# Kernel optimization log

Measured on AMD Instinct MI355X. Metric: run time of the kernel, lower is better.

Reference implementation:

```python
import jax, jax.numpy as jnp
import numpy as np

EPS = 1e-5


def _bn(h, gamma, beta):
    # BatchNorm1d, training mode: biased batch statistics over nodes
    mu = jnp.mean(h, axis=0)
    var = jnp.mean(jnp.square(h - mu), axis=0)
    return (h - mu) * jax.lax.rsqrt(var + EPS) * gamma + beta


def setup_inputs() -> dict:
    key = jax.random.key(0)
    ks = jax.random.split(key, 12)
    N, E, D, H = 50000, 800000, 128, 256
    x = jax.random.normal(ks[0], (N, D), dtype=jnp.float32)
    edge_index = jax.random.randint(ks[1], (2, E), 0, N, dtype=jnp.int64)
    train_node_id = jax.random.randint(ks[2], (10000,), 0, N, dtype=jnp.int64)
    def lin(k, fan_in, fan_out):
        bound = 1.0 / np.sqrt(fan_in)
        return jax.random.uniform(k, (fan_in, fan_out), jnp.float32, -bound, bound)
    return {
        "x": x, "edge_index": edge_index, "train_node_id": train_node_id,
        "W1": lin(ks[3], D, H), "b1": jnp.zeros((H,), jnp.float32),
        "W2": lin(ks[4], H, H), "b2": jnp.zeros((H,), jnp.float32),
        "W3": lin(ks[5], H, H), "b3": jnp.zeros((H,), jnp.float32),
        "g1": jnp.ones((H,), jnp.float32), "be1": jnp.zeros((H,), jnp.float32),
        "g2": jnp.ones((H,), jnp.float32), "be2": jnp.zeros((H,), jnp.float32),
        "g3": jnp.ones((H,), jnp.float32), "be3": jnp.zeros((H,), jnp.float32),
        "Wl": lin(ks[6], H, H), "bl": jnp.zeros((H,), jnp.float32),
        "Wf": lin(ks[7], H, 1), "bf": jnp.zeros((1,), jnp.float32),
    }


def reference(x, edge_index, train_node_id, W1, b1, W2, b2, W3, b3,
              g1, be1, g2, be2, g3, be3, Wl, bl, Wf, bf):
    N = x.shape[0]
    loops = jnp.arange(N, dtype=edge_index.dtype)
    row = jnp.concatenate([edge_index[0], loops])  # destinations
    col = jnp.concatenate([edge_index[1], loops])  # sources
    deg = jax.ops.segment_sum(jnp.ones_like(row, dtype=x.dtype), row, num_segments=N)
    d_isqrt = jax.lax.rsqrt(deg)  # deg >= 1 due to self loops
    norm = (d_isqrt[row] * d_isqrt[col])[:, None]  # [E+N, 1]

    def gcn(h, W, b):
        hW = h @ W
        agg = jax.ops.segment_sum(hW[col] * norm, row, num_segments=N)
        return agg + b

    h = jax.nn.relu(_bn(gcn(x, W1, b1), g1, be1))
    h = jax.nn.relu(_bn(gcn(h, W2, b2), g2, be2))
    h = jax.nn.relu(_bn(gcn(h, W3, b3), g3, be3))
    h = jax.nn.relu(h @ Wl + bl)
    h = h[train_node_id]
    return jnp.squeeze(h @ Wf + bf, -1)
```

## Files before the change

### kernel.cpp

```cpp
#include <hip/hip_runtime.h>

typedef unsigned short u16;
typedef unsigned char u8;
typedef __attribute__((ext_vector_type(8))) short short8;
typedef __attribute__((ext_vector_type(4))) float f32x4;

#define GPB 25
#define SCAP 8

#define DEVFN static __device__ __forceinline__

DEVFN u16 f2b(float f) {
    union { float f; unsigned v; } x; x.f = f;
    unsigned r = x.v + 0x7fffu + ((x.v >> 16) & 1u);
    return (u16)(r >> 16);
}

DEVFN int detect64(const int* __restrict__ p) {
    int orv = 0;
#pragma unroll
    for (int i = 1; i < 64; i += 2) orv |= p[i];
    return (orv == 0) ? 1 : 0;
}

DEVFN unsigned get_xcc() {
    unsigned x;
    asm volatile("s_getreg_b32 %0, hwreg(HW_REG_XCC_ID)" : "=s"(x));
    return x & 7u;
}

DEVFN void accum_row8(short8 v, float* acc) {
    const unsigned* u = (const unsigned*)&v;
#pragma unroll
    for (int k = 0; k < 4; k++) {
        union { float f; unsigned w; } lo, hi;
        lo.w = u[k] << 16;
        hi.w = u[k] & 0xffff0000u;
        acc[2 * k] += lo.f;
        acc[2 * k + 1] += hi.f;
    }
}

__global__ void k_init(const float* __restrict__ W1, const float* __restrict__ W2,
                       const float* __restrict__ W3, const float* __restrict__ Wl,
                       u16* __restrict__ T1, u16* __restrict__ T2,
                       u16* __restrict__ T3, u16* __restrict__ Tl,
                       int* __restrict__ z9,
                       float* __restrict__ stat, float* __restrict__ out, int N, int M) {
    int t = blockIdx.x * 256 + threadIdx.x;
    int Z = (N * 9) / 4;
    if (t < 229376) {
        const float* W; u16* T; int K; int idx;
        if (t < 32768)        { W = W1; T = T1; K = 128; idx = t; }
        else if (t < 98304)   { W = W2; T = T2; K = 256; idx = t - 32768; }
        else if (t < 163840)  { W = W3; T = T3; K = 256; idx = t - 98304; }
        else                  { W = Wl; T = Tl; K = 256; idx = t - 163840; }
        int k = idx >> 8, n = idx & 255;
        T[(size_t)n * K + k] = f2b(W[(size_t)k * 256 + n]);
    } else if (t < 229376 + Z) {
        ((int4*)z9)[t - 229376] = (int4){0, 0, 0, 0};
    } else if (t < 229376 + Z + 384) {
        ((float4*)stat)[t - 229376 - Z] = (float4){0.f, 0.f, 0.f, 0.f};
    } else if (t < 229376 + Z + 384 + (M + 3) / 4) {
        int i = (t - 229376 - Z - 384) * 4;
        if (i + 3 < M) *(float4*)(out + i) = (float4){0.f, 0.f, 0.f, 0.f};
        else for (int k = i; k < M; k++) out[k] = 0.f;
    }
}

__global__ void k_fill(const int* __restrict__ ei, unsigned* __restrict__ cntp,
                       int* __restrict__ ovfc, u16* __restrict__ slotp,
                       u16* __restrict__ ovf, int E, int N) {
    int fl = detect64(ei);
    unsigned xcc = get_xcc();
    size_t pbase = (size_t)xcc * N;
    int t = blockIdx.x * 256 + threadIdx.x;
    int e0 = t * 2;
    if (e0 >= E) return;
    int r0, r1, c0, c1;
    bool two = (e0 + 1 < E);
    if (fl) {
        const int4* p4 = (const int4*)ei;
        int4 d = p4[t];
        int4 s = p4[(E >> 1) + t];
        r0 = d.x; r1 = d.z; c0 = s.x; c1 = s.z;
    } else {
        const int2* p2 = (const int2*)ei;
        int2 d = p2[t];
        int2 s = p2[(E >> 1) + t];
        r0 = d.x; r1 = d.y; c0 = s.x; c1 = s.y;
    }
    {
        unsigned p = __hip_atomic_fetch_add(&cntp[pbase + r0], 1u,
                                            __ATOMIC_RELAXED, __HIP_MEMORY_SCOPE_WORKGROUP);
        if (p < SCAP) slotp[(pbase + r0) * SCAP + p] = (u16)c0;
        else { int q = atomicAdd(&ovfc[r0], 1); if (q < 64) ovf[(size_t)r0 * 64 + q] = (u16)c0; }
    }
    if (two) {
        unsigned p = __hip_atomic_fetch_add(&cntp[pbase + r1], 1u,
                                            __ATOMIC_RELAXED, __HIP_MEMORY_SCOPE_WORKGROUP);
        if (p < SCAP) slotp[(pbase + r1) * SCAP + p] = (u16)c1;
        else { int q = atomicAdd(&ovfc[r1], 1); if (q < 64) ovf[(size_t)r1 * 64 + q] = (u16)c1; }
    }
}

__global__ __launch_bounds__(256) void k_prep(
        const unsigned* __restrict__ cntp, const int* __restrict__ ovfc,
        const u16* __restrict__ slotp, int* __restrict__ cnt,
        u16* __restrict__ slots, u16* __restrict__ ovf,
        const float* __restrict__ x, float* __restrict__ disq,
        u16* __restrict__ xb, int N, int CB) {
    int b = blockIdx.x;
    if (b < CB) {
        int lane = threadIdx.x & 63;
        int wv = threadIdx.x >> 6;
        int ns = lane >> 3;
        int sh = lane & 7;
        int d = b * 32 + wv * 8 + ns;
        if (d >= N) return;
        size_t po = (size_t)sh * N + d;
        int craw = (int)cntp[po];
        int cl = min(craw, SCAP);
        short8 cell = *(const short8*)(slotp + po * SCAP);
        const u16* ep = (const u16*)&cell;
        int s = cl;
#pragma unroll
        for (int i = 1; i < 8; i <<= 1) {
            int v = __shfl_up(s, i, 64);
            if (sh >= i) s += v;
        }
        int P = s - cl;
        int avail = __shfl(s, lane | 7, 64);
        int spilled = min(ovfc[d], 64);
        u16* sd = slots + (size_t)d * 32;
        u16* ovp = ovf + (size_t)d * 64;
#pragma unroll
        for (int i = 0; i < SCAP; i++) {
            if (i < cl) {
                int pos = P + i;
                u16 val = ep[i];
                if (pos < 32) sd[pos] = val;
                else { int qq = spilled + pos - 32; if (qq < 64) ovp[qq] = val; }
            }
        }
        if (sh == 7) {
            int selfpos = avail;
            if (selfpos < 32) sd[selfpos] = (u16)d;
            else { int qq = spilled + selfpos - 32; if (qq < 64) ovp[qq] = (u16)d; }
            int dc = min(avail + 1, 32);
            int tot = min(avail + 1 + spilled, dc + 64);
            cnt[d] = dc | (tot << 8);
        }
    } else {
        int tt = (b - CB) * 256 + threadIdx.x;
        if (tt >= N * 32) return;
        int row = tt >> 5;
        int l = tt & 31;
        int s = (l < 8) ? (int)cntp[(size_t)l * N + row] : 0;
        s += __shfl_xor(s, 1, 64);
        s += __shfl_xor(s, 2, 64);
        s += __shfl_xor(s, 4, 64);
        s += __shfl_xor(s, 8, 64);
        s += __shfl_xor(s, 16, 64);
        float dq = rsqrtf((float)(s + 1));
        if (l == 0) disq[row] = dq;
        int f0 = l * 4;
        float4 vx = *(const float4*)(x + (size_t)row * 128 + f0);
        ushort4 o;
        o.x = f2b(vx.x * dq); o.y = f2b(vx.y * dq); o.z = f2b(vx.z * dq); o.w = f2b(vx.w * dq);
        *(ushort4*)(xb + (size_t)(f0 >> 5) * N * 32 + (size_t)row * 32 + (f0 & 31)) = o;
    }
}

template<int PBITS>
__global__ __launch_bounds__(256) void k_gatherP(
        const u16* __restrict__ src, const int* __restrict__ cnt,
        const u16* __restrict__ slots, const u16* __restrict__ ovf,
        const float* __restrict__ disq, u16* __restrict__ dst, int N) {
    const int NP = 1 << PBITS;
    const size_t N32 = (size_t)N * 32;
    int plane = blockIdx.x & (NP - 1);
    int lane = threadIdx.x & 63;
    int wv = threadIdx.x >> 6;
    int j = lane >> 2;
    int piece = lane & 3;
    int dbase = (blockIdx.x >> PBITS) * 64 + wv * 16;
    int d = dbase + j;
    bool live = d < N;
    int packed = live ? cnt[d] : 0;
    int dc = packed & 0xff;
    int tot = packed >> 8;
    float di = live ? disq[d] : 0.f;

    short8 sb = *(const short8*)(slots + (size_t)dbase * 32 + lane * 8);
    const unsigned* sbw = (const unsigned*)&sb;

    const u16* sbase = src + (size_t)plane * N32 + piece * 8;
    const u16* ov = ovf + (size_t)d * 64;

    float acc[8] = {0.f, 0.f, 0.f, 0.f, 0.f, 0.f, 0.f, 0.f};

    int m = dc;
    m = max(m, __shfl_xor(m, 4, 64));
    m = max(m, __shfl_xor(m, 8, 64));
    m = max(m, __shfl_xor(m, 16, 64));
    m = max(m, __shfl_xor(m, 32, 64));

    for (int rb = 0; rb < 4; rb++) {
        int r0 = rb * 8;
        if (r0 >= m) break;
        int srcl = j * 4 + rb;
        int cs[8];
#pragma unroll
        for (int rw = 0; rw < 4; rw++) {
            unsigned w = (unsigned)__shfl((int)sbw[rw], srcl, 64);
#pragma unroll
            for (int hh = 0; hh < 2; hh++) {
                int r = r0 + rw * 2 + hh;
                u16 s = hh ? (u16)(w >> 16) : (u16)(w & 0xffffu);
                cs[rw * 2 + hh] = (r < dc) ? (int)s : -1;
            }
        }
        short8 vs[8];
#pragma unroll
        for (int k = 0; k < 8; k++)
            if (cs[k] >= 0) vs[k] = *(const short8*)(sbase + (size_t)cs[k] * 32);
#pragma unroll
        for (int k = 0; k < 8; k++)
            if (cs[k] >= 0) accum_row8(vs[k], acc);
    }

    int nov = tot - dc;
    int novm = nov;
    novm = max(novm, __shfl_xor(novm, 4, 64));
    novm = max(novm, __shfl_xor(novm, 8, 64));
    novm = max(novm, __shfl_xor(novm, 16, 64));
    novm = max(novm, __shfl_xor(novm, 32, 64));
    for (int r = 0; r < novm; r++) {
        if (r < nov) {
            int c = (int)ov[r];
            short8 v = *(const short8*)(sbase + (size_t)c * 32);
            accum_row8(v, acc);
        }
    }

    if (live) {
        short8 o;
        u16* op = (u16*)&o;
#pragma unroll
        for (int k = 0; k < 8; k++) op[k] = f2b(acc[k] * di);
        __builtin_nontemporal_store(o,
            (short8*)(dst + (size_t)plane * N32 + (size_t)d * 32 + piece * 8));
    }
}

template<int KS>
__global__ __launch_bounds__(256, 2) void k_gemm_rb(
        const u16* __restrict__ A, const u16* __restrict__ Wt,
        float* __restrict__ Cf, int PS, int Gtot,
        float* __restrict__ stat, const float* __restrict__ bias,
        const float* __restrict__ Wfp, const float* __restrict__ bfp,
        float* __restrict__ outp) {
    constexpr int K = KS * 32;
    __shared__ float sbuf[4][2][64];
    int wv = threadIdx.x >> 6;
    int lane = threadIdx.x & 63;
    int quad = lane >> 4;
    int mr = lane & 15;
    int colbase = blockIdx.y * 64;
    int g0 = blockIdx.x * GPB;

    short8 Bf[4][KS];
#pragma unroll
    for (int j = 0; j < 4; j++)
#pragma unroll
        for (int s = 0; s < KS; s++)
            Bf[j][s] = *(const short8*)(Wt + (size_t)(colbase + j * 16 + mr) * K + s * 32 + quad * 8);

    float4 bv4[4], wf4[4];
    if (Wfp) {
#pragma unroll
        for (int j = 0; j < 4; j++) {
            bv4[j] = *(const float4*)(bias + colbase + j * 16 + quad * 4);
            wf4[j] = *(const float4*)(Wfp + colbase + j * 16 + quad * 4);
        }
    }

    f32x4 sreg[4], s2reg[4];
#pragma unroll
    for (int j = 0; j < 4; j++) {
        sreg[j] = (f32x4){0.f, 0.f, 0.f, 0.f};
        s2reg[j] = (f32x4){0.f, 0.f, 0.f, 0.f};
    }

    for (int g = wv; g < GPB; g += 4) {
        int gg = g0 + g;
        if (gg >= Gtot) continue;
        int row = gg * 16 + mr;
        const u16* Ap = A + (size_t)row * 32 + quad * 8;

        short8 Af[KS];
#pragma unroll
        for (int s = 0; s < KS; s++) Af[s] = *(const short8*)(Ap + (size_t)s * PS);

        f32x4 acc[4];
#pragma unroll
        for (int j = 0; j < 4; j++) acc[j] = (f32x4){0.f, 0.f, 0.f, 0.f};
#pragma unroll
        for (int s = 0; s < KS; s++)
#pragma unroll
            for (int j = 0; j < 4; j++)
                acc[j] = __builtin_amdgcn_mfma_f32_16x16x32_bf16(Bf[j][s], Af[s], acc[j], 0, 0, 0);

        if (Wfp) {
            float pr = 0.f;
#pragma unroll
            for (int j = 0; j < 4; j++) {
                const float* bj = (const float*)&bv4[j];
                const float* wj = (const float*)&wf4[j];
#pragma unroll
                for (int r = 0; r < 4; r++) {
                    float v = fmaxf(acc[j][r] + bj[r], 0.f);
                    pr += v * wj[r];
                }
            }
            pr += __shfl_xor(pr, 16, 64);
            pr += __shfl_xor(pr, 32, 64);
            if (quad == 0) {
                float v = pr;
                if (blockIdx.y == 0) v += bfp[0];
                atomicAdd(&outp[row], v);
            }
            continue;
        }

        float* cp = Cf + (size_t)row * 256 + colbase + quad * 4;
#pragma unroll
        for (int j = 0; j < 4; j++) {
            *(f32x4*)(cp + j * 16) = acc[j];
            sreg[j] += acc[j];
            s2reg[j] += acc[j] * acc[j];
        }
    }

    if (stat) {
#pragma unroll
        for (int j = 0; j < 4; j++) {
#pragma unroll
            for (int r = 0; r < 4; r++) {
                float a = sreg[j][r], b = s2reg[j][r];
                a += __shfl_xor(a, 1, 64); b += __shfl_xor(b, 1, 64);
                a += __shfl_xor(a, 2, 64); b += __shfl_xor(b, 2, 64);
                a += __shfl_xor(a, 4, 64); b += __shfl_xor(b, 4, 64);
                a += __shfl_xor(a, 8, 64); b += __shfl_xor(b, 8, 64);
                if (mr == 0) {
                    sbuf[wv][0][j * 16 + quad * 4 + r] = a;
                    sbuf[wv][1][j * 16 + quad * 4 + r] = b;
                }
            }
        }
        __syncthreads();
        int t = threadIdx.x;
        if (t < 128) {
            int which = t >> 6, c = t & 63;
            float v = sbuf[0][which][c] + sbuf[1][which][c] +
                      sbuf[2][which][c] + sbuf[3][which][c];
            atomicAdd(&stat[which * 256 + colbase + c], v);
        }
    }
}


__global__ void k_bnapply(const float* __restrict__ t, const float* __restrict__ stat,
                          const float* __restrict__ gamma, const float* __restrict__ beta,
                          u16* __restrict__ h, int N, float invN,
                          const float* __restrict__ scale) {
    size_t tt = (size_t)blockIdx.x * 256 + threadIdx.x;
    size_t base = tt * 4;
    if (base >= (size_t)N * 256) return;
    int f0 = (int)(base & 255);
    int row = (int)(base >> 8);
    float sc2 = scale ? scale[row] : 1.0f;
    float4 v = *(const float4*)(t + base);
    float r[4] = {v.x, v.y, v.z, v.w};
    ushort4 o;
    u16* op = (u16*)&o;
#pragma unroll
    for (int j = 0; j < 4; j++) {
        int f = f0 + j;
        float mean = stat[f] * invN;
        float var = stat[256 + f] * invN - mean * mean;
        float rstd = rsqrtf(var + 1e-5f);
        float sc = rstd * gamma[f];
        float sh = beta[f] - mean * sc;
        op[j] = f2b(fmaxf(r[j] * sc + sh, 0.0f) * sc2);
    }
    *(ushort4*)(h + (size_t)(f0 >> 5) * N * 32 + (size_t)row * 32 + (f0 & 31)) = o;
}

__global__ void k_bnapply_idx(const float* __restrict__ t, const float* __restrict__ stat,
                              const float* __restrict__ gamma, const float* __restrict__ beta,
                              const int* __restrict__ idx, u16* __restrict__ zin,
                              int M, float invN) {
    int fl = detect64(idx);
    size_t tt = (size_t)blockIdx.x * 256 + threadIdx.x;
    size_t base = tt * 4;
    if (base >= (size_t)M * 256) return;
    int f0 = (int)(base & 255);
    int row = (int)(base >> 8);
    int node = idx[(size_t)row << fl];
    float4 v = *(const float4*)(t + (size_t)node * 256 + f0);
    float r[4] = {v.x, v.y, v.z, v.w};
    ushort4 o;
    u16* op = (u16*)&o;
#pragma unroll
    for (int j = 0; j < 4; j++) {
        int f = f0 + j;
        float mean = stat[f] * invN;
        float var = stat[256 + f] * invN - mean * mean;
        float rstd = rsqrtf(var + 1e-5f);
        float sc = rstd * gamma[f];
        float sh = beta[f] - mean * sc;
        op[j] = f2b(fmaxf(r[j] * sc + sh, 0.0f));
    }
    *(ushort4*)(zin + (size_t)(f0 >> 5) * M * 32 + (size_t)row * 32 + (f0 & 31)) = o;
}


extern "C" void kernel_launch(void* const* d_in, const int* in_sizes, int n_in,
                              void* d_out, int out_size, void* d_ws, size_t ws_size,
                              hipStream_t stream) {
    const int D = 128, H = 256;
    const int N = in_sizes[0] / D;
    const int E = in_sizes[1] / 2;
    const int M = in_sizes[2];

    const float* x = (const float*)d_in[0];
    const int* ei = (const int*)d_in[1];
    const int* tnid = (const int*)d_in[2];
    const float* W1 = (const float*)d_in[3];
    const float* W2 = (const float*)d_in[5];
    const float* W3 = (const float*)d_in[7];
    const float* g1 = (const float*)d_in[9];
    const float* be1 = (const float*)d_in[10];
    const float* g2 = (const float*)d_in[11];
    const float* be2 = (const float*)d_in[12];
    const float* g3 = (const float*)d_in[13];
    const float* be3 = (const float*)d_in[14];
    const float* Wl = (const float*)d_in[15];
    const float* bl = (const float*)d_in[16];
    const float* Wf = (const float*)d_in[17];
    const float* bfp = (const float*)d_in[18];
    float* out = (float*)d_out;

    char* w = (char*)d_ws;
    size_t off = 0;
    auto carve = [&](size_t bytes) -> void* {
        void* p = w + off;
        off = (off + bytes + 255) & ~(size_t)255;
        return p;
    };

    float* stat = (float*)carve(3 * 512 * 4);
    float* disq = (float*)carve((size_t)N * 4);
    int* cnt = (int*)carve((size_t)N * 4);
    u16* slots = (u16*)carve((size_t)N * 32 * 2);
    u16* ovf = (u16*)carve((size_t)N * 64 * 2);
    u16* Wt1 = (u16*)carve((size_t)H * D * 2);
    u16* Wt2 = (u16*)carve((size_t)H * H * 2);
    u16* Wt3 = (u16*)carve((size_t)H * H * 2);
    u16* Wtl = (u16*)carve((size_t)H * H * 2);
    u16* xb = (u16*)carve((size_t)N * D * 2);
    u16* aggx = (u16*)carve((size_t)N * D * 2);
    u16* aggh = (u16*)carve((size_t)N * H * 2);
    float* tb = (float*)carve((size_t)N * H * 4);
    u16* hb = (u16*)carve((size_t)N * H * 2);
    u16* zin = (u16*)carve((size_t)M * H * 2);

    unsigned* cntp = (unsigned*)tb;
    int* ovfc = (int*)(cntp + (size_t)8 * N);
    u16* slotp = (u16*)(ovfc + N);

    const float invN = 1.0f / (float)N;

    const int Gn = N / 16;
    const int Gm = M / 16;
    dim3 gemm_grid((Gn + GPB - 1) / GPB, 4);
    dim3 gemm_grid_m((Gm + GPB - 1) / GPB, 4);
    const int PSn = N * 32;
    const int PSm = M * 32;
    const int chunks = (N + 63) / 64;
    const int PB = (int)(((size_t)N * H / 4 + 255) / 256);
    const int PBm = (int)(((size_t)M * H / 4 + 255) / 256);
    const int CB = (N + 31) / 32;
    const int XB = (N * 32 + 255) / 256;
    const int initT = 229376 + (N * 9) / 4 + 384 + (M + 3) / 4;

    k_init<<<(initT + 255) / 256, 256, 0, stream>>>(
        W1, W2, W3, Wl, Wt1, Wt2, Wt3, Wtl, (int*)cntp, stat, out, N, M);
    k_fill<<<(E / 2 + 255) / 256, 256, 0, stream>>>(ei, cntp, ovfc, slotp, ovf, E, N);
    k_prep<<<CB + XB, 256, 0, stream>>>(cntp, ovfc, slotp, cnt, slots, ovf, x, disq, xb, N, CB);

    k_gatherP<2><<<4 * chunks, 256, 0, stream>>>(xb, cnt, slots, ovf, disq, aggx, N);
    k_gemm_rb<4><<<gemm_grid, 256, 0, stream>>>(aggx, Wt1, tb, PSn, Gn, stat, nullptr, nullptr, nullptr, nullptr);
    k_bnapply<<<PB, 256, 0, stream>>>(tb, stat, g1, be1, hb, N, invN, disq);
    k_gatherP<3><<<8 * chunks, 256, 0, stream>>>(hb, cnt, slots, ovf, disq, aggh, N);
    k_gemm_rb<8><<<gemm_grid, 256, 0, stream>>>(aggh, Wt2, tb, PSn, Gn, stat + 512, nullptr, nullptr, nullptr, nullptr);
    k_bnapply<<<PB, 256, 0, stream>>>(tb, stat + 512, g2, be2, hb, N, invN, disq);
    k_gatherP<3><<<8 * chunks, 256, 0, stream>>>(hb, cnt, slots, ovf, disq, aggh, N);
    k_gemm_rb<8><<<gemm_grid, 256, 0, stream>>>(aggh, Wt3, tb, PSn, Gn, stat + 1024, nullptr, nullptr, nullptr, nullptr);
    k_bnapply_idx<<<PBm, 256, 0, stream>>>(tb, stat + 1024, g3, be3, tnid, zin, M, invN);

    k_gemm_rb<8><<<gemm_grid_m, 256, 0, stream>>>(zin, Wtl, nullptr, PSm, Gm, nullptr, bl, Wf, bfp, out);
}
```

Before: 401.4 us.

## Sort destination nodes by degree for gather balance and prefetch GEMM A tiles

Buckets destination nodes by in-degree (33 keys, 16 sub-buckets to spread atomics) via count, prefix-scan and scatter kernels, producing a permutation that the gather kernels follow so the lanes of a wavefront have similar neighbour counts and less loop divergence. The gather now reads slots and writes outputs at scattered node rows instead of contiguous ones. Separately, the GEMM kernel software-prefetches the next A fragment group into registers while computing the current one. Costs are two extra small launches, more register pressure in the GEMM, and less memory locality in the gather.

```diff
diff --git a/kernel.cpp b/kernel.cpp
--- a/kernel.cpp
+++ b/kernel.cpp
@@ -7,6 +7,9 @@
 
 #define GPB 25
 #define SCAP 8
+#define NKEY 33
+#define NSUB 16
+#define NBUK (NKEY * NSUB)
 
 #define DEVFN static __device__ __forceinline__
 
@@ -48,7 +51,7 @@
                        int* __restrict__ z9,
                        float* __restrict__ stat, float* __restrict__ out, int N, int M) {
     int t = blockIdx.x * 256 + threadIdx.x;
-    int Z = (N * 9) / 4;
+    int Z = (N * 9 + NBUK) / 4;
     if (t < 229376) {
         const float* W; u16* T; int K; int idx;
         if (t < 32768)        { W = W1; T = T1; K = 128; idx = t; }
@@ -107,7 +110,7 @@
 __global__ __launch_bounds__(256) void k_prep(
         const unsigned* __restrict__ cntp, const int* __restrict__ ovfc,
         const u16* __restrict__ slotp, int* __restrict__ cnt,
-        u16* __restrict__ slots, u16* __restrict__ ovf,
+        u16* __restrict__ slots, u16* __restrict__ ovf, int* __restrict__ bcnt,
         const float* __restrict__ x, float* __restrict__ disq,
         u16* __restrict__ xb, int N, int CB) {
     int b = blockIdx.x;
@@ -150,6 +153,8 @@
             int dc = min(avail + 1, 32);
             int tot = min(avail + 1 + spilled, dc + 64);
             cnt[d] = dc | (tot << 8);
+            int key = (tot > dc) ? 32 : (dc - 1);
+            atomicAdd(&bcnt[key * NSUB + (d & (NSUB - 1))], 1);
         }
     } else {
         int tt = (b - CB) * 256 + threadIdx.x;
@@ -172,11 +177,47 @@
     }
 }
 
+__global__ void k_pfx(const int* __restrict__ bcnt, int* __restrict__ bbase) {
+    int lane = threadIdx.x;
+    const int PER = 9;
+    int v[PER]; int s = 0;
+#pragma unroll
+    for (int i = 0; i < PER; i++) {
+        int idx = lane * PER + i;
+        v[i] = (idx < NBUK) ? bcnt[idx] : 0;
+        s += v[i];
+    }
+    int incl = s;
+#pragma unroll
+    for (int i = 1; i < 64; i <<= 1) {
+        int t = __shfl_up(incl, i, 64);
+        if (lane >= i) incl += t;
+    }
+    int run = incl - s;
+#pragma unroll
+    for (int i = 0; i < PER; i++) {
+        int idx = lane * PER + i;
+        if (idx < NBUK) { bbase[idx] = run; run += v[i]; }
+    }
+}
+
+__global__ void k_scatter(const int* __restrict__ cnt, int* __restrict__ bbase,
+                          int* __restrict__ perm, int N) {
+    int d = blockIdx.x * 256 + threadIdx.x;
+    if (d >= N) return;
+    int packed = cnt[d];
+    int dc = packed & 0xff, tot = packed >> 8;
+    int key = (tot > dc) ? 32 : (dc - 1);
+    int pos = atomicAdd(&bbase[key * NSUB + (d & (NSUB - 1))], 1);
+    perm[pos] = d;
+}
+
 template<int PBITS>
 __global__ __launch_bounds__(256) void k_gatherP(
         const u16* __restrict__ src, const int* __restrict__ cnt,
         const u16* __restrict__ slots, const u16* __restrict__ ovf,
-        const float* __restrict__ disq, u16* __restrict__ dst, int N) {
+        const float* __restrict__ disq, const int* __restrict__ perm,
+        u16* __restrict__ dst, int N) {
     const int NP = 1 << PBITS;
     const size_t N32 = (size_t)N * 32;
     int plane = blockIdx.x & (NP - 1);
@@ -184,19 +225,19 @@
     int wv = threadIdx.x >> 6;
     int j = lane >> 2;
     int piece = lane & 3;
-    int dbase = (blockIdx.x >> PBITS) * 64 + wv * 16;
-    int d = dbase + j;
-    bool live = d < N;
-    int packed = live ? cnt[d] : 0;
+    int idx0 = (blockIdx.x >> PBITS) * 64 + wv * 16 + j;
+    bool live = idx0 < N;
+    int pd = live ? perm[idx0] : 0;
+    int packed = live ? cnt[pd] : 0;
     int dc = packed & 0xff;
     int tot = packed >> 8;
-    float di = live ? disq[d] : 0.f;
-
-    short8 sb = *(const short8*)(slots + (size_t)dbase * 32 + lane * 8);
+    float di = live ? disq[pd] : 0.f;
+
+    short8 sb = *(const short8*)(slots + (size_t)pd * 32 + piece * 8);
     const unsigned* sbw = (const unsigned*)&sb;
 
     const u16* sbase = src + (size_t)plane * N32 + piece * 8;
-    const u16* ov = ovf + (size_t)d * 64;
+    const u16* ov = ovf + (size_t)pd * 64;
 
     float acc[8] = {0.f, 0.f, 0.f, 0.f, 0.f, 0.f, 0.f, 0.f};
 
@@ -250,7 +291,7 @@
 #pragma unroll
         for (int k = 0; k < 8; k++) op[k] = f2b(acc[k] * di);
         __builtin_nontemporal_store(o,
-            (short8*)(dst + (size_t)plane * N32 + (size_t)d * 32 + piece * 8));
+            (short8*)(dst + (size_t)plane * N32 + (size_t)pd * 32 + piece * 8));
     }
 }
 
@@ -293,15 +334,28 @@
         s2reg[j] = (f32x4){0.f, 0.f, 0.f, 0.f};
     }
 
+    short8 Afc[KS];
+    {
+        const u16* Ap = A + (size_t)((g0 + wv) * 16 + mr) * 32 + quad * 8;
+#pragma unroll
+        for (int s = 0; s < KS; s++) Afc[s] = *(const short8*)(Ap + (size_t)s * PS);
+    }
+
     for (int g = wv; g < GPB; g += 4) {
         int gg = g0 + g;
-        if (gg >= Gtot) continue;
+        if (gg >= Gtot) break;
         int row = gg * 16 + mr;
-        const u16* Ap = A + (size_t)row * 32 + quad * 8;
-
-        short8 Af[KS];
-#pragma unroll
-        for (int s = 0; s < KS; s++) Af[s] = *(const short8*)(Ap + (size_t)s * PS);
+
+        short8 Afn[KS];
+        int gn = g + 4;
+        if (gn < GPB) {
+            const u16* Ap = A + (size_t)((g0 + gn) * 16 + mr) * 32 + quad * 8;
+#pragma unroll
+            for (int s = 0; s < KS; s++) Afn[s] = *(const short8*)(Ap + (size_t)s * PS);
+        } else {
+#pragma unroll
+            for (int s = 0; s < KS; s++) Afn[s] = Afc[s];
+        }
 
         f32x4 acc[4];
 #pragma unroll
@@ -310,7 +364,7 @@
         for (int s = 0; s < KS; s++)
 #pragma unroll
             for (int j = 0; j < 4; j++)
-                acc[j] = __builtin_amdgcn_mfma_f32_16x16x32_bf16(Bf[j][s], Af[s], acc[j], 0, 0, 0);
+                acc[j] = __builtin_amdgcn_mfma_f32_16x16x32_bf16(Bf[j][s], Afc[s], acc[j], 0, 0, 0);
 
         if (Wfp) {
             float pr = 0.f;
@@ -331,16 +385,18 @@
                 if (blockIdx.y == 0) v += bfp[0];
                 atomicAdd(&outp[row], v);
             }
-            continue;
-        }
-
-        float* cp = Cf + (size_t)row * 256 + colbase + quad * 4;
-#pragma unroll
-        for (int j = 0; j < 4; j++) {
-            *(f32x4*)(cp + j * 16) = acc[j];
-            sreg[j] += acc[j];
-            s2reg[j] += acc[j] * acc[j];
-        }
+        } else {
+            float* cp = Cf + (size_t)row * 256 + colbase + quad * 4;
+#pragma unroll
+            for (int j = 0; j < 4; j++) {
+                *(f32x4*)(cp + j * 16) = acc[j];
+                sreg[j] += acc[j];
+                s2reg[j] += acc[j] * acc[j];
+            }
+        }
+
+#pragma unroll
+        for (int s = 0; s < KS; s++) Afc[s] = Afn[s];
     }
 
     if (stat) {
@@ -476,10 +532,13 @@
     float* tb = (float*)carve((size_t)N * H * 4);
     u16* hb = (u16*)carve((size_t)N * H * 2);
     u16* zin = (u16*)carve((size_t)M * H * 2);
+    int* perm = (int*)carve((size_t)N * 4);
+    int* bbase = (int*)carve(NBUK * 4);
 
     unsigned* cntp = (unsigned*)tb;
     int* ovfc = (int*)(cntp + (size_t)8 * N);
-    u16* slotp = (u16*)(ovfc + N);
+    int* bcnt = ovfc + N;
+    u16* slotp = (u16*)(bcnt + NBUK);
 
     const float invN = 1.0f / (float)N;
 
@@ -494,20 +553,22 @@
     const int PBm = (int)(((size_t)M * H / 4 + 255) / 256);
     const int CB = (N + 31) / 32;
     const int XB = (N * 32 + 255) / 256;
-    const int initT = 229376 + (N * 9) / 4 + 384 + (M + 3) / 4;
+    const int initT = 229376 + (N * 9 + NBUK) / 4 + 384 + (M + 3) / 4;
 
     k_init<<<(initT + 255) / 256, 256, 0, stream>>>(
         W1, W2, W3, Wl, Wt1, Wt2, Wt3, Wtl, (int*)cntp, stat, out, N, M);
     k_fill<<<(E / 2 + 255) / 256, 256, 0, stream>>>(ei, cntp, ovfc, slotp, ovf, E, N);
-    k_prep<<<CB + XB, 256, 0, stream>>>(cntp, ovfc, slotp, cnt, slots, ovf, x, disq, xb, N, CB);
-
-    k_gatherP<2><<<4 * chunks, 256, 0, stream>>>(xb, cnt, slots, ovf, disq, aggx, N);
+    k_prep<<<CB + XB, 256, 0, stream>>>(cntp, ovfc, slotp, cnt, slots, ovf, bcnt, x, disq, xb, N, CB);
+    k_pfx<<<1, 64, 0, stream>>>(bcnt, bbase);
+    k_scatter<<<(N + 255) / 256, 256, 0, stream>>>(cnt, bbase, perm, N);
+
+    k_gatherP<2><<<4 * chunks, 256, 0, stream>>>(xb, cnt, slots, ovf, disq, perm, aggx, N);
     k_gemm_rb<4><<<gemm_grid, 256, 0, stream>>>(aggx, Wt1, tb, PSn, Gn, stat, nullptr, nullptr, nullptr, nullptr);
     k_bnapply<<<PB, 256, 0, stream>>>(tb, stat, g1, be1, hb, N, invN, disq);
-    k_gatherP<3><<<8 * chunks, 256, 0, stream>>>(hb, cnt, slots, ovf, disq, aggh, N);
+    k_gatherP<3><<<8 * chunks, 256, 0, stream>>>(hb, cnt, slots, ovf, disq, perm, aggh, N);
     k_gemm_rb<8><<<gemm_grid, 256, 0, stream>>>(aggh, Wt2, tb, PSn, Gn, stat + 512, nullptr, nullptr, nullptr, nullptr);
     k_bnapply<<<PB, 256, 0, stream>>>(tb, stat + 512, g2, be2, hb, N, invN, disq);
-    k_gatherP<3><<<8 * chunks, 256, 0, stream>>>(hb, cnt, slots, ovf, disq, aggh, N);
+    k_gatherP<3><<<8 * chunks, 256, 0, stream>>>(hb, cnt, slots, ovf, disq, perm, aggh, N);
     k_gemm_rb<8><<<gemm_grid, 256, 0, stream>>>(aggh, Wt3, tb, PSn, Gn, stat + 1024, nullptr, nullptr, nullptr, nullptr);
     k_bnapply_idx<<<PBm, 256, 0, stream>>>(tb, stat + 1024, g3, be3, tnid, zin, M, invN);
 
```

After: 534.4 us. +33.1%, slower.
